# Kernel optimization log

Measured on AMD Instinct MI355X. Metric: run time of the kernel, lower is better.

The kernel has to match this reference:

```python
import jax, jax.numpy as jnp
import numpy as np

LOOKUP_WINDOW = 101  # module init arg
EPS = 1e-12  # F.normalize eps


def setup_inputs() -> dict:
    key = jax.random.key(0)
    k1, k2, k3 = jax.random.split(key, 3)
    B, T, F_IN, D = 4, 2048, 2048, 128
    x = jax.random.normal(k1, (B, T, F_IN), dtype=jnp.float32)
    # nn.Linear(in_filters, output_dim); stored here as [in, out] so y = x @ W + b
    W = jax.random.normal(k2, (F_IN, D), dtype=jnp.float32) / np.sqrt(F_IN).astype(np.float32)
    b = jax.random.normal(k3, (D,), dtype=jnp.float32) * 0.01
    return {"x": x, "W": W, "b": b}


def reference(x, W, b):
    hw = LOOKUP_WINDOW // 2
    # projection + L2 normalize over feature dim (F.normalize p=2, dim=-1)
    p = x @ W + b  # [B,T,D]
    p = p / jnp.maximum(jnp.linalg.norm(p, axis=-1, keepdims=True), EPS)
    B, T, D = p.shape
    # zero-pad along time so out-of-range neighbors contribute 0 similarity
    pp = jnp.pad(p, ((0, 0), (hw, hw), (0, 0)))  # [B, T+2*hw, D]
    # window gather: idx[t, w] = t + w indexes padded time axis (neighbor t + w - hw)
    idx = jnp.arange(T)[:, None] + jnp.arange(LOOKUP_WINDOW)[None, :]  # [T, W]
    windows = pp[:, idx, :]  # [B, T, W, D]
    # banded similarity: sim[b,t,w] = <p[b,t], neighbor at offset w-hw>
    sim = jnp.einsum('btd,btwd->btw', p, windows)
    return sim  # [B, T, LOOKUP_WINDOW]
```

## Files before the change

### kernel.cpp

```cpp
#include <hip/hip_runtime.h>
#include <hip/hip_bf16.h>

#define T_LEN 2048
#define D_DIM 128
#define K_DIM 2048
#define M_DIM 8192
#define LOOKUP 101
#define HWIN 50

typedef __attribute__((ext_vector_type(8))) short short8;
typedef __attribute__((ext_vector_type(4))) float f32x4;

static __device__ __forceinline__ unsigned int f2bf(float f) {
  unsigned int u = __float_as_uint(f);
  return (u + 0x7fffu + ((u >> 16) & 1u)) >> 16;
}

static __device__ __forceinline__ short8 pack8(float4 lo, float4 hi) {
  uint4 u;
  u.x = f2bf(lo.x) | (f2bf(lo.y) << 16);
  u.y = f2bf(lo.z) | (f2bf(lo.w) << 16);
  u.z = f2bf(hi.x) | (f2bf(hi.y) << 16);
  u.w = f2bf(hi.z) | (f2bf(hi.w) << 16);
  return *(short8*)&u;
}

__global__ __launch_bounds__(256) void k_pack(const float* __restrict__ W,
                                              unsigned short* __restrict__ Bp) {
  __shared__ float sw[32][132];
  const int ks = blockIdx.x;
  const int t = threadIdx.x;
  const float* src = W + (size_t)ks * 32 * D_DIM;
#pragma unroll
  for (int j = 0; j < 4; ++j) {
    int idx = t + j * 256;
    int row = idx >> 5, c4 = idx & 31;
    float4 v = *(const float4*)(src + row * D_DIM + c4 * 4);
    *(float4*)&sw[row][c4 * 4] = v;
  }
  __syncthreads();
#pragma unroll
  for (int e = 0; e < 2; ++e) {
    int f = t * 2 + e;
    int ct = f >> 6, l = f & 63;
    int kr = (l >> 4) * 8, col = ct * 16 + (l & 15);
    uint4 o;
    o.x = f2bf(sw[kr + 0][col]) | (f2bf(sw[kr + 1][col]) << 16);
    o.y = f2bf(sw[kr + 2][col]) | (f2bf(sw[kr + 3][col]) << 16);
    o.z = f2bf(sw[kr + 4][col]) | (f2bf(sw[kr + 5][col]) << 16);
    o.w = f2bf(sw[kr + 6][col]) | (f2bf(sw[kr + 7][col]) << 16);
    *(uint4*)(Bp + (((size_t)(ks * 8 + ct) << 6) + l) * 8) = o;
  }
}

__global__ __launch_bounds__(512, 2) void k_gemm(const float* __restrict__ X,
                                                 const unsigned short* __restrict__ Bp,
                                                 const float* __restrict__ bias,
                                                 unsigned short* __restrict__ Pn) {
  __shared__ __align__(16) unsigned char Pw[4 * 16384];
  const int tid = threadIdx.x;
  const int lane = tid & 63;
  const int wv = tid >> 6;
  const int r0 = blockIdx.x * 32;
  const int l15 = lane & 15;
  const int kg = lane >> 4;

  const float* xb0 = X + (size_t)(r0 + l15) * K_DIM + wv * 256 + kg * 8;
  const float* xb1 = xb0 + (size_t)16 * K_DIM;

  f32x4 acc[2][8];
#pragma unroll
  for (int g = 0; g < 2; ++g)
#pragma unroll
    for (int i = 0; i < 8; ++i) acc[g][i] = (f32x4){0.f, 0.f, 0.f, 0.f};

  float4 xc[2][2], xn[2][2];
  short8 wc[8], wn[8];

  xc[0][0] = *(const float4*)(xb0);
  xc[0][1] = *(const float4*)(xb0 + 4);
  xc[1][0] = *(const float4*)(xb1);
  xc[1][1] = *(const float4*)(xb1 + 4);
#pragma unroll
  for (int ct = 0; ct < 8; ++ct)
    wc[ct] = *(const short8*)(Bp + (((size_t)(wv * 8) * 8 + ct) * 64 + lane) * 8);

#pragma unroll
  for (int s = 0; s < 8; ++s) {
    if (s < 7) {
      xn[0][0] = *(const float4*)(xb0 + (s + 1) * 32);
      xn[0][1] = *(const float4*)(xb0 + (s + 1) * 32 + 4);
      xn[1][0] = *(const float4*)(xb1 + (s + 1) * 32);
      xn[1][1] = *(const float4*)(xb1 + (s + 1) * 32 + 4);
#pragma unroll
      for (int ct = 0; ct < 8; ++ct)
        wn[ct] = *(const short8*)(Bp + (((size_t)(wv * 8 + s + 1) * 8 + ct) * 64 + lane) * 8);
    }
    short8 xf0 = pack8(xc[0][0], xc[0][1]);
    short8 xf1 = pack8(xc[1][0], xc[1][1]);
#pragma unroll
    for (int ct = 0; ct < 8; ++ct)
      acc[0][ct] = __builtin_amdgcn_mfma_f32_16x16x32_bf16(wc[ct], xf0, acc[0][ct], 0, 0, 0);
#pragma unroll
    for (int ct = 0; ct < 8; ++ct)
      acc[1][ct] = __builtin_amdgcn_mfma_f32_16x16x32_bf16(wc[ct], xf1, acc[1][ct], 0, 0, 0);
    if (s < 7) {
      xc[0][0] = xn[0][0]; xc[0][1] = xn[0][1];
      xc[1][0] = xn[1][0]; xc[1][1] = xn[1][1];
#pragma unroll
      for (int ct = 0; ct < 8; ++ct) wc[ct] = wn[ct];
    }
  }

  if (wv >= 4) {
    unsigned char* pb = Pw + (wv - 4) * 16384;
#pragma unroll
    for (int rg = 0; rg < 2; ++rg)
#pragma unroll
      for (int ct = 0; ct < 8; ++ct) {
        int byte = (rg * 16 + l15) * 512 + ((ct * 64 + kg * 16) ^ ((l15 & 7) << 4));
        *(float4*)(pb + byte) = make_float4(acc[rg][ct][0], acc[rg][ct][1], acc[rg][ct][2], acc[rg][ct][3]);
      }
  }
  __syncthreads();
  if (wv < 4) {
    unsigned char* pb = Pw + wv * 16384;
#pragma unroll
    for (int rg = 0; rg < 2; ++rg)
#pragma unroll
      for (int ct = 0; ct < 8; ++ct) {
        int byte = (rg * 16 + l15) * 512 + ((ct * 64 + kg * 16) ^ ((l15 & 7) << 4));
        float4 v = *(float4*)(pb + byte);
        v.x += acc[rg][ct][0]; v.y += acc[rg][ct][1];
        v.z += acc[rg][ct][2]; v.w += acc[rg][ct][3];
        *(float4*)(pb + byte) = v;
      }
  }
  __syncthreads();

  const int row = tid >> 4;
  const int c8 = tid & 15;
  float tot[8];
#pragma unroll
  for (int i = 0; i < 8; ++i) tot[i] = 0.f;
#pragma unroll
  for (int q = 0; q < 4; ++q)
#pragma unroll
    for (int h = 0; h < 2; ++h) {
      int byte = q * 16384 + row * 512 + (((c8 * 32 + h * 16)) ^ ((row & 7) << 4));
      float4 v = *(const float4*)(Pw + byte);
      tot[h * 4 + 0] += v.x; tot[h * 4 + 1] += v.y;
      tot[h * 4 + 2] += v.z; tot[h * 4 + 3] += v.w;
    }
  float4 bv0 = *(const float4*)(bias + c8 * 8);
  float4 bv1 = *(const float4*)(bias + c8 * 8 + 4);
  tot[0] += bv0.x; tot[1] += bv0.y; tot[2] += bv0.z; tot[3] += bv0.w;
  tot[4] += bv1.x; tot[5] += bv1.y; tot[6] += bv1.z; tot[7] += bv1.w;
  float ss = 0.f;
#pragma unroll
  for (int i = 0; i < 8; ++i) ss += tot[i] * tot[i];
  ss += __shfl_xor(ss, 1);
  ss += __shfl_xor(ss, 2);
  ss += __shfl_xor(ss, 4);
  ss += __shfl_xor(ss, 8);
  float sc = 1.0f / fmaxf(sqrtf(ss), 1e-12f);
  uint4 o;
  o.x = f2bf(tot[0] * sc) | (f2bf(tot[1] * sc) << 16);
  o.y = f2bf(tot[2] * sc) | (f2bf(tot[3] * sc) << 16);
  o.z = f2bf(tot[4] * sc) | (f2bf(tot[5] * sc) << 16);
  o.w = f2bf(tot[6] * sc) | (f2bf(tot[7] * sc) << 16);
  *(uint4*)(Pn + (size_t)(r0 + row) * D_DIM + c8 * 8) = o;
}

#define SROWS 144

__global__ __launch_bounds__(256) void k_sim(const unsigned short* __restrict__ Pn,
                                             float* __restrict__ out) {
  __shared__ unsigned short sm[SROWS * D_DIM];
  const int bb = blockIdx.x >> 6;
  const int tb = blockIdx.x & 63;
  const int t0 = tb * 32;
  const int tid = threadIdx.x;

  for (int idx = tid; idx < SROWS * 16; idx += 256) {
    int i = idx >> 4, seg = idx & 15;
    int t = t0 - HWIN + i;
    uint4 val = make_uint4(0u, 0u, 0u, 0u);
    if (t >= 0 && t < T_LEN)
      val = *(const uint4*)(Pn + ((size_t)bb * T_LEN + t) * D_DIM + seg * 8);
    *(uint4*)&sm[i * D_DIM + ((seg ^ (i & 7)) << 3)] = val;
  }
  __syncthreads();

  const int lane = tid & 63;
  const int wv = tid >> 6;
  const int l15 = lane & 15;
  const int kg = lane >> 4;
  const int rt = wv >> 1;
  const int itp = wv & 1;

  short8 af[4];
  const int ia = HWIN + rt * 16 + l15;
#pragma unroll
  for (int ks = 0; ks < 4; ++ks) {
    int g = ks * 4 + kg;
    af[ks] = *(const short8*)&sm[ia * D_DIM + ((g ^ (ia & 7)) << 3)];
  }

  for (int it = itp; it < 9; it += 2) {
    f32x4 acc = (f32x4){0.f, 0.f, 0.f, 0.f};
    const int ib = it * 16 + l15;
#pragma unroll
    for (int ks = 0; ks < 4; ++ks) {
      int g = ks * 4 + kg;
      short8 bf = *(const short8*)&sm[ib * D_DIM + ((g ^ (ib & 7)) << 3)];
      acc = __builtin_amdgcn_mfma_f32_16x16x32_bf16(af[ks], bf, acc, 0, 0, 0);
    }
#pragma unroll
    for (int j = 0; j < 4; ++j) {
      int r = rt * 16 + kg * 4 + j;
      int w = ib - r;
      if (w >= 0 && w <= 100)
        out[((size_t)bb * T_LEN + t0 + r) * LOOKUP + w] = acc[j];
    }
  }
}

extern "C" void kernel_launch(void* const* d_in, const int* in_sizes, int n_in,
                              void* d_out, int out_size, void* d_ws, size_t ws_size,
                              hipStream_t stream) {
  (void)in_sizes; (void)n_in; (void)out_size; (void)ws_size;
  const float* x = (const float*)d_in[0];
  const float* W = (const float*)d_in[1];
  const float* b = (const float*)d_in[2];
  float* out = (float*)d_out;
  unsigned short* Bp = (unsigned short*)d_ws;
  unsigned short* Pn = Bp + (size_t)D_DIM * K_DIM;

  k_pack<<<64, 256, 0, stream>>>(W, Bp);
  k_gemm<<<M_DIM / 32, 512, 0, stream>>>(x, Bp, b, Pn);
  k_sim<<<4 * (T_LEN / 32), 256, 0, stream>>>(Pn, out);
}
```

Baseline: 32.91 us.

## Warp-specialize GEMM with producer waves streaming X via global_load_lds ring

Splits the GEMM block into two producer waves that stream X tiles directly into a 12-slot LDS ring with global_load_lds, and six consumer waves that read those tiles, convert them to bf16 and run the MFMAs. The waves coordinate through volatile LDS flags and spin-waits. The cross-wave reduction now sums six partial tiles through the reused ring buffer instead of four. It aims to decouple memory latency from compute, at the cost of only six MFMA waves, spin-wait overhead, and larger LDS use (96KB ring), which may limit occupancy to one block per CU.

```diff
diff --git a/kernel.cpp b/kernel.cpp
--- a/kernel.cpp
+++ b/kernel.cpp
@@ -23,6 +23,12 @@
   u.z = f2bf(hi.x) | (f2bf(hi.y) << 16);
   u.w = f2bf(hi.z) | (f2bf(hi.w) << 16);
   return *(short8*)&u;
+}
+
+typedef __attribute__((address_space(3))) unsigned char lds_uchar;
+typedef const __attribute__((address_space(1))) unsigned char g_uchar;
+static __device__ __forceinline__ void gll16(const void* g, void* l) {
+  __builtin_amdgcn_global_load_lds((g_uchar*)g, (lds_uchar*)l, 16, 0, 0);
 }
 
 __global__ __launch_bounds__(256) void k_pack(const float* __restrict__ W,
@@ -53,11 +59,16 @@
   }
 }
 
+#define NCH 32
+#define RSL 12
+
 __global__ __launch_bounds__(512, 2) void k_gemm(const float* __restrict__ X,
                                                  const unsigned short* __restrict__ Bp,
                                                  const float* __restrict__ bias,
                                                  unsigned short* __restrict__ Pn) {
-  __shared__ __align__(16) unsigned char Pw[4 * 16384];
+  __shared__ __align__(16) unsigned char ring[RSL * 8192];
+  __shared__ int flg[NCH];
+  __shared__ int dn[NCH];
   const int tid = threadIdx.x;
   const int lane = tid & 63;
   const int wv = tid >> 6;
@@ -65,8 +76,10 @@
   const int l15 = lane & 15;
   const int kg = lane >> 4;
 
-  const float* xb0 = X + (size_t)(r0 + l15) * K_DIM + wv * 256 + kg * 8;
-  const float* xb1 = xb0 + (size_t)16 * K_DIM;
+  if (tid < NCH) { flg[tid] = 0; dn[tid] = 0; }
+  __syncthreads();
+  volatile int* vflg = flg;
+  volatile int* vdn = dn;
 
   f32x4 acc[2][8];
 #pragma unroll
@@ -74,66 +87,71 @@
 #pragma unroll
     for (int i = 0; i < 8; ++i) acc[g][i] = (f32x4){0.f, 0.f, 0.f, 0.f};
 
-  float4 xc[2][2], xn[2][2];
-  short8 wc[8], wn[8];
-
-  xc[0][0] = *(const float4*)(xb0);
-  xc[0][1] = *(const float4*)(xb0 + 4);
-  xc[1][0] = *(const float4*)(xb1);
-  xc[1][1] = *(const float4*)(xb1 + 4);
-#pragma unroll
-  for (int ct = 0; ct < 8; ++ct)
-    wc[ct] = *(const short8*)(Bp + (((size_t)(wv * 8) * 8 + ct) * 64 + lane) * 8);
-
-#pragma unroll
-  for (int s = 0; s < 8; ++s) {
-    if (s < 7) {
-      xn[0][0] = *(const float4*)(xb0 + (s + 1) * 32);
-      xn[0][1] = *(const float4*)(xb0 + (s + 1) * 32 + 4);
-      xn[1][0] = *(const float4*)(xb1 + (s + 1) * 32);
-      xn[1][1] = *(const float4*)(xb1 + (s + 1) * 32 + 4);
-#pragma unroll
-      for (int ct = 0; ct < 8; ++ct)
-        wn[ct] = *(const short8*)(Bp + (((size_t)(wv * 8 + s + 1) * 8 + ct) * 64 + lane) * 8);
-    }
-    short8 xf0 = pack8(xc[0][0], xc[0][1]);
-    short8 xf1 = pack8(xc[1][0], xc[1][1]);
-#pragma unroll
-    for (int ct = 0; ct < 8; ++ct)
-      acc[0][ct] = __builtin_amdgcn_mfma_f32_16x16x32_bf16(wc[ct], xf0, acc[0][ct], 0, 0, 0);
-#pragma unroll
-    for (int ct = 0; ct < 8; ++ct)
-      acc[1][ct] = __builtin_amdgcn_mfma_f32_16x16x32_bf16(wc[ct], xf1, acc[1][ct], 0, 0, 0);
-    if (s < 7) {
-      xc[0][0] = xn[0][0]; xc[0][1] = xn[0][1];
-      xc[1][0] = xn[1][0]; xc[1][1] = xn[1][1];
-#pragma unroll
-      for (int ct = 0; ct < 8; ++ct) wc[ct] = wn[ct];
-    }
-  }
-
-  if (wv >= 4) {
-    unsigned char* pb = Pw + (wv - 4) * 16384;
+  if (wv >= 6) {
+    const int p = wv - 6;
+    const int li = lane >> 4;
+    const int lg = lane & 15;
+    auto issue = [&](int c) {
+      unsigned char* slot = ring + (c % RSL) * 8192;
+#pragma unroll
+      for (int i = 0; i < 8; ++i) {
+        int r = 4 * i + li;
+        int g = lg ^ (r & 7);
+        const float* src = X + (size_t)(r0 + r) * K_DIM + c * 64 + g * 4;
+        gll16(src, slot + i * 1024);
+      }
+    };
+    issue(p);
+    for (int c = p; c < NCH; c += 2) {
+      if (c + 2 < NCH) {
+        if (c + 2 >= RSL) {
+          while (vdn[c + 2 - RSL] == 0) __builtin_amdgcn_s_sleep(1);
+        }
+        issue(c + 2);
+        asm volatile("s_waitcnt vmcnt(8)" ::: "memory");
+      } else {
+        asm volatile("s_waitcnt vmcnt(0)" ::: "memory");
+      }
+      if (lane == 0) vflg[c] = 1;
+    }
+  } else {
+    for (int c = wv; c < NCH; c += 6) {
+      while (vflg[c] == 0) __builtin_amdgcn_s_sleep(1);
+      const unsigned char* slot = ring + (c % RSL) * 8192;
+#pragma unroll
+      for (int s = 0; s < 2; ++s) {
+        short8 wc[8];
+        int ksg = c * 2 + s;
+#pragma unroll
+        for (int ct = 0; ct < 8; ++ct)
+          wc[ct] = *(const short8*)(Bp + (((size_t)ksg * 8 + ct) * 64 + lane) * 8);
+#pragma unroll
+        for (int rg = 0; rg < 2; ++rg) {
+          int r = rg * 16 + l15;
+          const unsigned char* rb = slot + (r >> 2) * 1024 + (r & 3) * 256;
+          int g0 = s * 8 + kg * 2;
+          float4 lo = *(const float4*)(rb + ((g0 ^ (r & 7)) << 4));
+          float4 hi = *(const float4*)(rb + (((g0 + 1) ^ (r & 7)) << 4));
+          short8 xf = pack8(lo, hi);
+#pragma unroll
+          for (int ct = 0; ct < 8; ++ct)
+            acc[rg][ct] = __builtin_amdgcn_mfma_f32_16x16x32_bf16(wc[ct], xf, acc[rg][ct], 0, 0, 0);
+        }
+      }
+      if (lane == 0) vdn[c] = 1;
+    }
+  }
+  __syncthreads();
+
+  if (wv < 6) {
+    unsigned char* pb = ring + wv * 16384;
 #pragma unroll
     for (int rg = 0; rg < 2; ++rg)
 #pragma unroll
       for (int ct = 0; ct < 8; ++ct) {
         int byte = (rg * 16 + l15) * 512 + ((ct * 64 + kg * 16) ^ ((l15 & 7) << 4));
-        *(float4*)(pb + byte) = make_float4(acc[rg][ct][0], acc[rg][ct][1], acc[rg][ct][2], acc[rg][ct][3]);
-      }
-  }
-  __syncthreads();
-  if (wv < 4) {
-    unsigned char* pb = Pw + wv * 16384;
-#pragma unroll
-    for (int rg = 0; rg < 2; ++rg)
-#pragma unroll
-      for (int ct = 0; ct < 8; ++ct) {
-        int byte = (rg * 16 + l15) * 512 + ((ct * 64 + kg * 16) ^ ((l15 & 7) << 4));
-        float4 v = *(float4*)(pb + byte);
-        v.x += acc[rg][ct][0]; v.y += acc[rg][ct][1];
-        v.z += acc[rg][ct][2]; v.w += acc[rg][ct][3];
-        *(float4*)(pb + byte) = v;
+        *(float4*)(pb + byte) =
+            make_float4(acc[rg][ct][0], acc[rg][ct][1], acc[rg][ct][2], acc[rg][ct][3]);
       }
   }
   __syncthreads();
@@ -144,11 +162,11 @@
 #pragma unroll
   for (int i = 0; i < 8; ++i) tot[i] = 0.f;
 #pragma unroll
-  for (int q = 0; q < 4; ++q)
+  for (int q = 0; q < 6; ++q)
 #pragma unroll
     for (int h = 0; h < 2; ++h) {
-      int byte = q * 16384 + row * 512 + (((c8 * 32 + h * 16)) ^ ((row & 7) << 4));
-      float4 v = *(const float4*)(Pw + byte);
+      int byte = q * 16384 + row * 512 + ((c8 * 32 + h * 16) ^ ((row & 7) << 4));
+      float4 v = *(const float4*)(ring + byte);
       tot[h * 4 + 0] += v.x; tot[h * 4 + 1] += v.y;
       tot[h * 4 + 2] += v.z; tot[h * 4 + 3] += v.w;
     }
```

Result: slower. 37.16 us (+12.9%).
